# Performance work log

Measured on AMD Instinct MI355X. Metric: run time of the kernel, lower is better.

The kernel has to match this reference:

```python
import jax, jax.numpy as jnp
import numpy as np

HEADS = 16  # matches init_kwargs


def setup_inputs() -> dict:
    key = jax.random.key(0)
    ks = jax.random.split(key, 9)
    N, L, E, D = 2, 2048, 1024, 64
    return {
        "query": jax.random.normal(ks[0], (N, L, E), dtype=jnp.float32),
        "keys": jax.random.normal(ks[1], (N, L, E), dtype=jnp.float32),
        "values": jax.random.normal(ks[2], (N, L, E), dtype=jnp.float32),
        "masks": jax.random.randint(ks[3], (N, 1, 1, L), 0, 2, dtype=jnp.int32),
        "Wq": jax.random.normal(ks[4], (D, D), dtype=jnp.float32) / np.sqrt(D),
        "Wk": jax.random.normal(ks[5], (D, D), dtype=jnp.float32) / np.sqrt(D),
        "Wv": jax.random.normal(ks[6], (D, D), dtype=jnp.float32) / np.sqrt(D),
        "Wo": jax.random.normal(ks[7], (E, E), dtype=jnp.float32) / np.sqrt(E),
        "bo": jax.random.normal(ks[8], (E,), dtype=jnp.float32),
    }


def reference(query, keys, values, masks, Wq, Wk, Wv, Wo, bo):
    N, Lq, E = query.shape
    Lk = keys.shape[1]
    H = HEADS
    D = E // H
    # split heads: [N, L, H, D]
    q = query.reshape(N, Lq, H, D)
    k = keys.reshape(N, Lk, H, D)
    v = values.reshape(N, Lk, H, D)
    # per-head linear projections (weights shared across heads); Linear: x @ W.T
    q = jnp.einsum("nqhd,ed->nqhe", q, Wq)
    k = jnp.einsum("nkhd,ed->nkhe", k, Wk)
    v = jnp.einsum("nkhd,ed->nkhe", v, Wv)
    # scores [N, H, Lq, Lk]
    scores = jnp.einsum("nqhd,nkhd->nhqk", q, k)
    scores = jnp.where(masks == 0, jnp.float32(-1e20), scores)
    # NOTE: original scales by sqrt(embed_size), not sqrt(head_dim)
    attn = jax.nn.softmax(scores / jnp.sqrt(jnp.float32(E)), axis=3)
    out = jnp.einsum("nhqk,nkhd->nqhd", attn, v).reshape(N, Lq, E)
    return out @ Wo.T + bo
```

## Files before the change

### kernel.cpp

```cpp
#include <hip/hip_runtime.h>


typedef __bf16 bf16_t;
typedef __bf16 bf16x4 __attribute__((ext_vector_type(4)));
typedef __bf16 bf16x8 __attribute__((ext_vector_type(8)));
typedef float f32x4 __attribute__((ext_vector_type(4)));
typedef unsigned int u32x4 __attribute__((ext_vector_type(4)));

#define MFMA16(a, b, c) __builtin_amdgcn_mfma_f32_16x16x32_bf16((a), (b), (c), 0, 0, 0)

#define GLOAD_LDS16(gp, lp)                                              \
    __builtin_amdgcn_global_load_lds(                                    \
        (const __attribute__((address_space(1))) void*)(gp),             \
        (__attribute__((address_space(3))) void*)(lp), 16, 0, 0)

__device__ inline bf16x8 cvt8(const float* __restrict__ p, float scale) {
    f32x4 a = *(const f32x4*)p;
    f32x4 b = *(const f32x4*)(p + 4);
    bf16x8 r;
    r[0] = (bf16_t)(a[0] * scale); r[1] = (bf16_t)(a[1] * scale);
    r[2] = (bf16_t)(a[2] * scale); r[3] = (bf16_t)(a[3] * scale);
    r[4] = (bf16_t)(b[0] * scale); r[5] = (bf16_t)(b[1] * scale);
    r[6] = (bf16_t)(b[2] * scale); r[7] = (bf16_t)(b[3] * scale);
    return r;
}

__device__ inline bf16x8 cvt8s(const f32x4 a, const f32x4 b, float scale) {
    bf16x8 r;
    r[0] = (bf16_t)(a[0] * scale); r[1] = (bf16_t)(a[1] * scale);
    r[2] = (bf16_t)(a[2] * scale); r[3] = (bf16_t)(a[3] * scale);
    r[4] = (bf16_t)(b[0] * scale); r[5] = (bf16_t)(b[1] * scale);
    r[6] = (bf16_t)(b[2] * scale); r[7] = (bf16_t)(b[3] * scale);
    return r;
}

__device__ inline float exp2_fast(float x) {
    float r;
    asm("v_exp_f32 %0, %1" : "=v"(r) : "v"(x));
    return r;
}

__device__ inline unsigned cvt_pk_bf16(float lo, float hi) {
    unsigned r;
    asm("v_cvt_pk_bf16_f32 %0, %1, %2" : "=v"(r) : "v"(lo), "v"(hi));
    return r;
}

__device__ inline void xchg_quads(unsigned &x, unsigned &y) {
    asm("v_permlane32_swap_b32 %0, %1\n\t"
        "v_permlane16_swap_b32 %0, %1"
        : "+v"(x), "+v"(y));
}

__global__ __launch_bounds__(256) void scan_kernel(const int* __restrict__ msk,
                                                   int* __restrict__ excl)
{
    __shared__ int wsum[4];
    const int n = blockIdx.x;
    const int t = threadIdx.x, lane = t & 63, w = t >> 6;
    const int* m = msk + n * 2048;
    int* e = excl + n * 2049;

    int v[8], s = 0;
    #pragma unroll
    for (int j = 0; j < 8; j++) { v[j] = (m[t * 8 + j] != 0); s += v[j]; }

    int inc = s;
    #pragma unroll
    for (int d = 1; d < 64; d <<= 1) {
        int o = __shfl_up(inc, d);
        if (lane >= d) inc += o;
    }
    if (lane == 63) wsum[w] = inc;
    __syncthreads();
    int off = 0;
    #pragma unroll
    for (int i = 0; i < 4; i++)
        if (i < w) off += wsum[i];

    int a = off + inc - s;
    #pragma unroll
    for (int j = 0; j < 8; j++) { e[t * 8 + j] = a; a += v[j]; }
    if (t == 255) e[2048] = a;
}

__global__ __launch_bounds__(256) void qkv_proj_kernel(
    const float* __restrict__ qin, const float* __restrict__ kin,
    const float* __restrict__ vin,
    const float* __restrict__ Wq, const float* __restrict__ Wk,
    const float* __restrict__ Wv, const float* __restrict__ Wo,
    const int* __restrict__ excl,
    bf16_t* __restrict__ qp, bf16_t* __restrict__ kc, bf16_t* __restrict__ vcT,
    bf16_t* __restrict__ Wob)
{
    __shared__ __align__(16) char smem[51200];

    const int t = threadIdx.x;
    const int w = t >> 6, lane = t & 63, quad = lane >> 4, l16 = lane & 15;

    if (blockIdx.y == 3) {
        int idx = blockIdx.x * 1024 + t * 4;
        f32x4 v = *(const f32x4*)&Wo[idx];
        bf16x4 r;
        r[0] = (bf16_t)v[0]; r[1] = (bf16_t)v[1];
        r[2] = (bf16_t)v[2]; r[3] = (bf16_t)v[3];
        *(bf16x4*)&Wob[idx] = r;
        return;
    }

    if (blockIdx.y == 2) {
        bf16_t* Ct = (bf16_t*)smem;
        short* mapS = (short*)(smem + 16384);
        const int h = blockIdx.x & 15;
        const int tb = (blockIdx.x >> 4) * 64;
        const int n = tb >> 11, l0 = tb & 2047;
        const int tg = tb + w * 16 + l16;

        bf16x8 b0 = cvt8(&vin[(size_t)tg * 1024 + h * 64 + quad * 8], 1.0f);
        bf16x8 b1 = cvt8(&vin[(size_t)tg * 1024 + h * 64 + 32 + quad * 8], 1.0f);

        const int cbase = excl[n * 2049 + l0];
        const int cnt   = excl[n * 2049 + l0 + 64] - cbase;
        if (t < 64) {
            int c  = excl[n * 2049 + l0 + t];
            int c1 = excl[n * 2049 + l0 + t + 1];
            if (c1 > c) mapS[c - cbase] = (short)t;
        }

        #pragma unroll
        for (int nt = 0; nt < 4; nt++) {
            bf16x8 a0 = cvt8(&Wv[(nt * 16 + l16) * 64 + quad * 8], 1.0f);
            bf16x8 a1 = cvt8(&Wv[(nt * 16 + l16) * 64 + 32 + quad * 8], 1.0f);
            f32x4 acc = {0.f, 0.f, 0.f, 0.f};
            acc = MFMA16(a0, b0, acc);
            acc = MFMA16(a1, b1, acc);
            #pragma unroll
            for (int r = 0; r < 4; r++)
                Ct[(nt * 16 + quad * 4 + r) * 72 + w * 16 + l16] = (bf16_t)acc[r];
        }
        __syncthreads();
        const int p = t & 63, rg = t >> 6;
        if (p < cnt) {
            int j = mapS[p];
            size_t ob = ((size_t)(n * 16 + h)) * 131072 + cbase + p;
            #pragma unroll
            for (int rr = 0; rr < 16; rr++) {
                int r = rg * 16 + rr;
                vcT[ob + (size_t)r * 2048] = Ct[r * 72 + j];
            }
        }
        return;
    }

    if (blockIdx.x >= 512) return;
    const bool isK = (blockIdx.y == 1);
    const float* x; const float* W; float scale;
    if (!isK) { x = qin; W = Wq; scale = 0.04508422f; }
    else      { x = kin; W = Wk; scale = 1.0f; }

    float* Xs = (float*)smem;
    bf16_t* Ct2 = (bf16_t*)(smem + 32768);

    const int g0 = blockIdx.x * 128;

    #pragma unroll
    for (int j = 0; j < 8; j++) {
        int br = w * 32 + j * 4;
        int srow = br + (lane >> 4);
        int scol = ((lane & 15) ^ (srow & 15)) * 4;
        GLOAD_LDS16(&x[(size_t)(g0 + srow) * 64 + scol], &Xs[br * 64]);
    }
    __syncthreads();

    const int rbase = w * 32;
    bf16x8 a[2][2];
    #pragma unroll
    for (int qs = 0; qs < 2; qs++) {
        int row = rbase + qs * 16 + l16;
        const char* rowp = (const char*)Xs + (size_t)row * 256;
        int swb = (row & 15) << 4;
        #pragma unroll
        for (int c = 0; c < 2; c++) {
            f32x4 lo = *(const f32x4*)(rowp + ((c * 128 + quad * 32) ^ swb));
            f32x4 hi = *(const f32x4*)(rowp + ((c * 128 + quad * 32 + 16) ^ swb));
            a[qs][c] = cvt8s(lo, hi, scale);
        }
    }

    f32x4 acc[4][2];
    #pragma unroll
    for (int nt = 0; nt < 4; nt++) {
        bf16x8 b0 = cvt8(&W[(nt * 16 + l16) * 64 + quad * 8], 1.0f);
        bf16x8 b1 = cvt8(&W[(nt * 16 + l16) * 64 + 32 + quad * 8], 1.0f);
        #pragma unroll
        for (int qs = 0; qs < 2; qs++) {
            f32x4 z = {0.f, 0.f, 0.f, 0.f};
            z = MFMA16(a[qs][0], b0, z);
            z = MFMA16(a[qs][1], b1, z);
            acc[nt][qs] = z;
        }
    }

    #pragma unroll
    for (int nt = 0; nt < 4; nt++)
        #pragma unroll
        for (int qs = 0; qs < 2; qs++)
            #pragma unroll
            for (int r = 0; r < 4; r++)
                Ct2[(rbase + qs * 16 + quad * 4 + r) * 72 + nt * 16 + l16] = (bf16_t)acc[nt][qs][r];
    __syncthreads();

    #pragma unroll
    for (int it = 0; it < 4; it++) {
        int j = it * 32 + (t >> 3);
        int g = g0 + j, h2 = g & 15, token = g >> 4;
        int n2 = token >> 11, l = token & 2047;
        bf16x8 val = *(const bf16x8*)&Ct2[j * 72 + (t & 7) * 8];
        if (isK) {
            int c  = excl[n2 * 2049 + l];
            int c1 = excl[n2 * 2049 + l + 1];
            if (c1 > c)
                *(bf16x8*)&kc[(((size_t)(n2 * 16 + h2)) * 2048 + c) * 64 + (t & 7) * 8] = val;
        } else {
            *(bf16x8*)&qp[(((size_t)(n2 * 16 + h2)) * 2048 + l) * 64 + (t & 7) * 8] = val;
        }
    }
}

__global__ __launch_bounds__(256) void attn_kernel(
    const bf16_t* __restrict__ qp, const bf16_t* __restrict__ kc,
    const bf16_t* __restrict__ vcT, const int* __restrict__ excl,
    bf16_t* __restrict__ ao)
{
    __shared__ bf16_t Kt[2][64][64];
    __shared__ bf16_t Vt[2][64][64];

    const int t = threadIdx.x;
    const int w = t >> 6, lane = t & 63, quad = lane >> 4, l16 = lane & 15;

    const int flat = blockIdx.x;
    const int xcd = flat & 7, slot = flat >> 3;
    const int nh = xcd * 4 + (slot >> 4), qb = slot & 15;
    const int n = nh >> 4, h = nh & 15;
    const int qbase = qb * 128 + w * 32;
    const size_t nhbase = (size_t)nh * 131072;

    const int Lc = excl[n * 2049 + 2048];
    const int ntiles = (Lc + 63) >> 6;

    const int scol = ((lane & 7) ^ (lane >> 3)) * 8;
    const int swr  = l16 & 7;
    const int ck0  = (quad ^ swr) * 8;
    const int ck1  = ((quad + 4) ^ swr) * 8;

    bf16x8 aq[2][2];
    #pragma unroll
    for (int qs = 0; qs < 2; qs++)
        #pragma unroll
        for (int c = 0; c < 2; c++)
            aq[qs][c] = *(const bf16x8*)&qp[nhbase + (size_t)(qbase + qs * 16 + l16) * 64 + c * 32 + quad * 8];

    f32x4 o[2][4];
    float lsum[2] = {0.f, 0.f};
    #pragma unroll
    for (int qs = 0; qs < 2; qs++)
        #pragma unroll
        for (int dt = 0; dt < 4; dt++) {
            o[qs][dt][0] = 0.f; o[qs][dt][1] = 0.f; o[qs][dt][2] = 0.f; o[qs][dt][3] = 0.f;
        }

    const int kwbase = w * 16;

    #pragma unroll
    for (int j = 0; j < 2; j++) {
        int rb = kwbase + j * 8;
        GLOAD_LDS16(&kc[nhbase + (size_t)(rb + (lane >> 3)) * 64 + scol], &Kt[0][rb][0]);
        GLOAD_LDS16(&vcT[nhbase + (size_t)(rb + (lane >> 3)) * 2048 + scol], &Vt[0][rb][0]);
    }

    for (int i = 0; i < ntiles; i++) {
        const int cb = i & 1, nb = cb ^ 1;
        const int k0 = i * 64;
        __syncthreads();

        if (i + 1 < ntiles) {
            const int kn = k0 + 64;
            #pragma unroll
            for (int j = 0; j < 2; j++) {
                int rb = kwbase + j * 8;
                GLOAD_LDS16(&kc[nhbase + (size_t)(kn + rb + (lane >> 3)) * 64 + scol],
                            &Kt[nb][rb][0]);
                GLOAD_LDS16(&vcT[nhbase + (size_t)(rb + (lane >> 3)) * 2048 + kn + scol],
                            &Vt[nb][rb][0]);
            }
        }

        f32x4 st[2][4];
        #pragma unroll
        for (int ct = 0; ct < 4; ct++) {
            bf16x8 kb0 = *(const bf16x8*)&Kt[cb][ct * 16 + l16][ck0];
            bf16x8 kb1 = *(const bf16x8*)&Kt[cb][ct * 16 + l16][ck1];
            #pragma unroll
            for (int qs = 0; qs < 2; qs++) {
                f32x4 acc = {0.f, 0.f, 0.f, 0.f};
                acc = MFMA16(kb0, aq[qs][0], acc);
                acc = MFMA16(kb1, aq[qs][1], acc);
                st[qs][ct] = acc;
            }
        }

        if (k0 + 64 <= Lc) {
            #pragma unroll
            for (int qs = 0; qs < 2; qs++)
                #pragma unroll
                for (int ct = 0; ct < 4; ct++)
                    #pragma unroll
                    for (int r = 0; r < 4; r++) {
                        float p = exp2_fast(st[qs][ct][r]);
                        lsum[qs] += p;
                        st[qs][ct][r] = p;
                    }
        } else {
            #pragma unroll
            for (int qs = 0; qs < 2; qs++)
                #pragma unroll
                for (int ct = 0; ct < 4; ct++)
                    #pragma unroll
                    for (int r = 0; r < 4; r++) {
                        int kk = k0 + ct * 16 + quad * 4 + r;
                        float p = (kk < Lc) ? exp2_fast(st[qs][ct][r]) : 0.0f;
                        lsum[qs] += p;
                        st[qs][ct][r] = p;
                    }
        }

        bf16x8 bp[2][2];
        #pragma unroll
        for (int qs = 0; qs < 2; qs++) {
            unsigned u[4][2];
            #pragma unroll
            for (int ct = 0; ct < 4; ct++) {
                u[ct][0] = cvt_pk_bf16(st[qs][ct][0], st[qs][ct][1]);
                u[ct][1] = cvt_pk_bf16(st[qs][ct][2], st[qs][ct][3]);
            }
            #pragma unroll
            for (int hh = 0; hh < 2; hh++) {
                unsigned b0 = u[2 * hh][0], b2 = u[2 * hh + 1][0];
                xchg_quads(b0, b2);
                unsigned b1 = u[2 * hh][1], b3 = u[2 * hh + 1][1];
                xchg_quads(b1, b3);
                u32x4 q4 = {b0, b1, b2, b3};
                bp[qs][hh] = __builtin_bit_cast(bf16x8, q4);
            }
        }

        #pragma unroll
        for (int dt = 0; dt < 4; dt++) {
            bf16x8 va0 = *(const bf16x8*)&Vt[cb][dt * 16 + l16][ck0];
            bf16x8 va1 = *(const bf16x8*)&Vt[cb][dt * 16 + l16][ck1];
            #pragma unroll
            for (int qs = 0; qs < 2; qs++) {
                o[qs][dt] = MFMA16(va0, bp[qs][0], o[qs][dt]);
                o[qs][dt] = MFMA16(va1, bp[qs][1], o[qs][dt]);
            }
        }
    }

    #pragma unroll
    for (int qs = 0; qs < 2; qs++) {
        float v = lsum[qs];
        v += __shfl_xor(v, 16);
        v += __shfl_xor(v, 32);
        float inv = 1.0f / v;
        const int q = qbase + qs * 16 + l16;
        const size_t base = ((size_t)n * 2048 + q) * 1024 + h * 64;
        #pragma unroll
        for (int dt = 0; dt < 4; dt++) {
            bf16x4 ov;
            #pragma unroll
            for (int r = 0; r < 4; r++) ov[r] = (bf16_t)(o[qs][dt][r] * inv);
            *(bf16x4*)&ao[base + dt * 16 + quad * 4] = ov;
        }
    }
}

__global__ __launch_bounds__(256, 2) void out_proj_kernel(
    const bf16_t* __restrict__ X, const bf16_t* __restrict__ Wob,
    const float* __restrict__ bo, float* __restrict__ out)
{
    __shared__ bf16_t Xs[2][128][64];
    __shared__ bf16_t Ws[2][64][64];

    const int t = threadIdx.x;
    const int w = t >> 6, lane = t & 63, quad = lane >> 4, l16 = lane & 15;
    const int Mbase = blockIdx.x * 128;
    const int Nbase = blockIdx.y * 64;
    const int mrow = (w & 1) * 64;
    const int ncol = (w >> 1) * 32;

    const int scol = ((lane & 7) ^ (lane >> 3)) * 8;
    const int swr  = l16 & 7;

    f32x4 acc[4][2];
    #pragma unroll
    for (int mi = 0; mi < 4; mi++)
        #pragma unroll
        for (int ni = 0; ni < 2; ni++) {
            acc[mi][ni][0] = 0.f; acc[mi][ni][1] = 0.f;
            acc[mi][ni][2] = 0.f; acc[mi][ni][3] = 0.f;
        }

    #pragma unroll
    for (int j = 0; j < 4; j++) {
        int br = w * 32 + j * 8;
        GLOAD_LDS16(&X[(size_t)(Mbase + br + (lane >> 3)) * 1024 + scol], &Xs[0][br][0]);
    }
    #pragma unroll
    for (int j = 0; j < 2; j++) {
        int br = w * 16 + j * 8;
        GLOAD_LDS16(&Wob[(size_t)(Nbase + br + (lane >> 3)) * 1024 + scol], &Ws[0][br][0]);
    }

    for (int i = 0; i < 16; i++) {
        const int cb = i & 1, nb = cb ^ 1;
        __syncthreads();

        if (i < 15) {
            const int kn = (i + 1) * 64;
            #pragma unroll
            for (int j = 0; j < 4; j++) {
                int br = w * 32 + j * 8;
                GLOAD_LDS16(&X[(size_t)(Mbase + br + (lane >> 3)) * 1024 + kn + scol],
                            &Xs[nb][br][0]);
            }
            #pragma unroll
            for (int j = 0; j < 2; j++) {
                int br = w * 16 + j * 8;
                GLOAD_LDS16(&Wob[(size_t)(Nbase + br + (lane >> 3)) * 1024 + kn + scol],
                            &Ws[nb][br][0]);
            }
        }

        #pragma unroll
        for (int c = 0; c < 2; c++) {
            bf16x8 bfr[2];
            #pragma unroll
            for (int ni = 0; ni < 2; ni++)
                bfr[ni] = *(const bf16x8*)&Ws[cb][ncol + ni * 16 + l16][((c * 4 + quad) ^ swr) * 8];
            #pragma unroll
            for (int mi = 0; mi < 4; mi++) {
                bf16x8 afr = *(const bf16x8*)&Xs[cb][mrow + mi * 16 + l16][((c * 4 + quad) ^ swr) * 8];
                #pragma unroll
                for (int ni = 0; ni < 2; ni++)
                    acc[mi][ni] = MFMA16(afr, bfr[ni], acc[mi][ni]);
            }
        }
    }

    #pragma unroll
    for (int ni = 0; ni < 2; ni++) {
        float b = bo[Nbase + ncol + ni * 16 + l16];
        #pragma unroll
        for (int mi = 0; mi < 4; mi++) {
            #pragma unroll
            for (int r = 0; r < 4; r++) {
                int row = Mbase + mrow + mi * 16 + quad * 4 + r;
                out[(size_t)row * 1024 + Nbase + ncol + ni * 16 + l16] = acc[mi][ni][r] + b;
            }
        }
    }
}

extern "C" void kernel_launch(void* const* d_in, const int* in_sizes, int n_in,
                              void* d_out, int out_size, void* d_ws, size_t ws_size,
                              hipStream_t stream)
{
    const float* qin = (const float*)d_in[0];
    const float* kin = (const float*)d_in[1];
    const float* vin = (const float*)d_in[2];
    const int*   msk = (const int*)d_in[3];
    const float* Wq  = (const float*)d_in[4];
    const float* Wk  = (const float*)d_in[5];
    const float* Wv  = (const float*)d_in[6];
    const float* Wo  = (const float*)d_in[7];
    const float* bo  = (const float*)d_in[8];
    float* out = (float*)d_out;

    bf16_t* ws  = (bf16_t*)d_ws;
    bf16_t* qp  = ws;
    bf16_t* kc  = ws + 4194304;
    bf16_t* vcT = ws + 8388608;
    bf16_t* ao  = ws + 12582912;
    bf16_t* Wob = ws + 16777216;
    int* excl   = (int*)(ws + 17825792);

    scan_kernel<<<2, 256, 0, stream>>>(msk, excl);
    qkv_proj_kernel<<<dim3(1024, 4), 256, 0, stream>>>(qin, kin, vin, Wq, Wk, Wv, Wo,
                                                        excl, qp, kc, vcT, Wob);
    attn_kernel<<<dim3(512), 256, 0, stream>>>(qp, kc, vcT, excl, ao);
    out_proj_kernel<<<dim3(32, 16), 256, 0, stream>>>(ao, Wob, bo, out);
}
```

Before: 173.5 us.

## Gather only unmasked keys via index map and widen attention KV tiles

```diff
diff --git a/kernel.cpp b/kernel.cpp
--- a/kernel.cpp
+++ b/kernel.cpp
@@ -53,13 +53,15 @@
 }
 
 __global__ __launch_bounds__(256) void scan_kernel(const int* __restrict__ msk,
-                                                   int* __restrict__ excl)
+                                                   int* __restrict__ excl,
+                                                   int* __restrict__ lmap)
 {
     __shared__ int wsum[4];
     const int n = blockIdx.x;
     const int t = threadIdx.x, lane = t & 63, w = t >> 6;
     const int* m = msk + n * 2048;
     int* e = excl + n * 2049;
+    int* lm = lmap + n * 2048;
 
     int v[8], s = 0;
     #pragma unroll
@@ -80,7 +82,11 @@
 
     int a = off + inc - s;
     #pragma unroll
-    for (int j = 0; j < 8; j++) { e[t * 8 + j] = a; a += v[j]; }
+    for (int j = 0; j < 8; j++) {
+        e[t * 8 + j] = a;
+        if (v[j]) lm[a] = t * 8 + j;
+        a += v[j];
+    }
     if (t == 255) e[2048] = a;
 }
 
@@ -89,7 +95,7 @@
     const float* __restrict__ vin,
     const float* __restrict__ Wq, const float* __restrict__ Wk,
     const float* __restrict__ Wv, const float* __restrict__ Wo,
-    const int* __restrict__ excl,
+    const int* __restrict__ excl, const int* __restrict__ lmap,
     bf16_t* __restrict__ qp, bf16_t* __restrict__ kc, bf16_t* __restrict__ vcT,
     bf16_t* __restrict__ Wob)
 {
@@ -110,22 +116,20 @@
 
     if (blockIdx.y == 2) {
         bf16_t* Ct = (bf16_t*)smem;
-        short* mapS = (short*)(smem + 16384);
         const int h = blockIdx.x & 15;
-        const int tb = (blockIdx.x >> 4) * 64;
-        const int n = tb >> 11, l0 = tb & 2047;
-        const int tg = tb + w * 16 + l16;
-
-        bf16x8 b0 = cvt8(&vin[(size_t)tg * 1024 + h * 64 + quad * 8], 1.0f);
-        bf16x8 b1 = cvt8(&vin[(size_t)tg * 1024 + h * 64 + 32 + quad * 8], 1.0f);
-
-        const int cbase = excl[n * 2049 + l0];
-        const int cnt   = excl[n * 2049 + l0 + 64] - cbase;
-        if (t < 64) {
-            int c  = excl[n * 2049 + l0 + t];
-            int c1 = excl[n * 2049 + l0 + t + 1];
-            if (c1 > c) mapS[c - cbase] = (short)t;
-        }
+        const int ctile = blockIdx.x >> 4;
+        const int n = ctile >> 5;
+        const int c0 = (ctile & 31) * 64;
+        const int Lc = excl[n * 2049 + 2048];
+        if (c0 >= Lc) return;
+
+        const int p0 = w * 16 + l16;
+        int cs = c0 + p0; if (cs > Lc - 1) cs = Lc - 1;
+        const int tg = lmap[n * 2048 + cs];
+        const size_t rb = ((size_t)(n * 2048 + tg)) * 1024 + h * 64;
+
+        bf16x8 b0 = cvt8(&vin[rb + quad * 8], 1.0f);
+        bf16x8 b1 = cvt8(&vin[rb + 32 + quad * 8], 1.0f);
 
         #pragma unroll
         for (int nt = 0; nt < 4; nt++) {
@@ -140,13 +144,13 @@
         }
         __syncthreads();
         const int p = t & 63, rg = t >> 6;
+        const int cnt = (Lc - c0 < 64) ? (Lc - c0) : 64;
         if (p < cnt) {
-            int j = mapS[p];
-            size_t ob = ((size_t)(n * 16 + h)) * 131072 + cbase + p;
+            size_t ob = ((size_t)(n * 16 + h)) * 131072 + c0 + p;
             #pragma unroll
             for (int rr = 0; rr < 16; rr++) {
                 int r = rg * 16 + rr;
-                vcT[ob + (size_t)r * 2048] = Ct[r * 72 + j];
+                vcT[ob + (size_t)r * 2048] = Ct[r * 72 + p];
             }
         }
         return;
@@ -155,8 +159,15 @@
     if (blockIdx.x >= 512) return;
     const bool isK = (blockIdx.y == 1);
     const float* x; const float* W; float scale;
+    int n = 0, c0 = 0, Lc = 0;
     if (!isK) { x = qin; W = Wq; scale = 0.04508422f; }
-    else      { x = kin; W = Wk; scale = 1.0f; }
+    else {
+        x = kin; W = Wk; scale = 1.0f;
+        n = blockIdx.x >> 8;
+        c0 = (blockIdx.x & 255) * 8;
+        Lc = excl[n * 2049 + 2048];
+        if (c0 >= Lc) return;
+    }
 
     float* Xs = (float*)smem;
     bf16_t* Ct2 = (bf16_t*)(smem + 32768);
@@ -168,7 +179,16 @@
         int br = w * 32 + j * 4;
         int srow = br + (lane >> 4);
         int scol = ((lane & 15) ^ (srow & 15)) * 4;
-        GLOAD_LDS16(&x[(size_t)(g0 + srow) * 64 + scol], &Xs[br * 64]);
+        size_t gaddr;
+        if (!isK) {
+            gaddr = (size_t)(g0 + srow) * 64 + scol;
+        } else {
+            int csx = c0 + (srow >> 4); if (csx > Lc - 1) csx = Lc - 1;
+            int hs = srow & 15;
+            int ls = lmap[n * 2048 + csx];
+            gaddr = ((size_t)((n * 2048 + ls) * 16 + hs)) * 64 + scol;
+        }
+        GLOAD_LDS16(&x[gaddr], &Xs[br * 64]);
     }
     __syncthreads();
 
@@ -213,15 +233,14 @@
     #pragma unroll
     for (int it = 0; it < 4; it++) {
         int j = it * 32 + (t >> 3);
-        int g = g0 + j, h2 = g & 15, token = g >> 4;
-        int n2 = token >> 11, l = token & 2047;
         bf16x8 val = *(const bf16x8*)&Ct2[j * 72 + (t & 7) * 8];
         if (isK) {
-            int c  = excl[n2 * 2049 + l];
-            int c1 = excl[n2 * 2049 + l + 1];
-            if (c1 > c)
-                *(bf16x8*)&kc[(((size_t)(n2 * 16 + h2)) * 2048 + c) * 64 + (t & 7) * 8] = val;
+            int c = c0 + (j >> 4), h2 = j & 15;
+            if (c < Lc)
+                *(bf16x8*)&kc[(((size_t)(n * 16 + h2)) * 2048 + c) * 64 + (t & 7) * 8] = val;
         } else {
+            int g = g0 + j, h2 = g & 15, token = g >> 4;
+            int n2 = token >> 11, l = token & 2047;
             *(bf16x8*)&qp[(((size_t)(n2 * 16 + h2)) * 2048 + l) * 64 + (t & 7) * 8] = val;
         }
     }
@@ -232,8 +251,8 @@
     const bf16_t* __restrict__ vcT, const int* __restrict__ excl,
     bf16_t* __restrict__ ao)
 {
-    __shared__ bf16_t Kt[2][64][64];
-    __shared__ bf16_t Vt[2][64][64];
+    __shared__ bf16_t Kt[2][128][64];
+    __shared__ bf16_t Vt[2][64][128];
 
     const int t = threadIdx.x;
     const int w = t >> 6, lane = t & 63, quad = lane >> 4, l16 = lane & 15;
@@ -246,12 +265,13 @@
     const size_t nhbase = (size_t)nh * 131072;
 
     const int Lc = excl[n * 2049 + 2048];
-    const int ntiles = (Lc + 63) >> 6;
-
-    const int scol = ((lane & 7) ^ (lane >> 3)) * 8;
-    const int swr  = l16 & 7;
-    const int ck0  = (quad ^ swr) * 8;
-    const int ck1  = ((quad + 4) ^ swr) * 8;
+    const int ntiles = (Lc + 127) >> 7;
+
+    const int ksrow = lane >> 3;
+    const int kscol = ((lane & 7) ^ (lane >> 3)) * 8;
+    const int swr = l16 & 7;
+    const int ck0 = (quad ^ swr) * 8;
+    const int ck1 = ((quad + 4) ^ swr) * 8;
 
     bf16x8 aq[2][2];
     #pragma unroll
@@ -269,100 +289,110 @@
             o[qs][dt][0] = 0.f; o[qs][dt][1] = 0.f; o[qs][dt][2] = 0.f; o[qs][dt][3] = 0.f;
         }
 
-    const int kwbase = w * 16;
-
-    #pragma unroll
-    for (int j = 0; j < 2; j++) {
-        int rb = kwbase + j * 8;
-        GLOAD_LDS16(&kc[nhbase + (size_t)(rb + (lane >> 3)) * 64 + scol], &Kt[0][rb][0]);
-        GLOAD_LDS16(&vcT[nhbase + (size_t)(rb + (lane >> 3)) * 2048 + scol], &Vt[0][rb][0]);
-    }
+#define STAGE_KV(buf, kn)                                                     \
+    {                                                                         \
+        _Pragma("unroll")                                                     \
+        for (int j = 0; j < 4; j++) {                                         \
+            int rb = w * 32 + j * 8;                                          \
+            GLOAD_LDS16(&kc[nhbase + (size_t)((kn) + rb + ksrow) * 64 + kscol],\
+                        &Kt[buf][rb][0]);                                     \
+        }                                                                     \
+        _Pragma("unroll")                                                     \
+        for (int j = 0; j < 4; j++) {                                         \
+            int rb = w * 16 + j * 4;                                          \
+            int d = rb + (lane >> 4);                                         \
+            int sc = ((lane & 15) ^ (d & 15)) * 8;                            \
+            GLOAD_LDS16(&vcT[nhbase + (size_t)d * 2048 + (kn) + sc],          \
+                        &Vt[buf][rb][0]);                                     \
+        }                                                                     \
+    }
+
+    STAGE_KV(0, 0);
 
     for (int i = 0; i < ntiles; i++) {
         const int cb = i & 1, nb = cb ^ 1;
-        const int k0 = i * 64;
+        const int k0 = i * 128;
         __syncthreads();
 
-        if (i + 1 < ntiles) {
-            const int kn = k0 + 64;
-            #pragma unroll
-            for (int j = 0; j < 2; j++) {
-                int rb = kwbase + j * 8;
-                GLOAD_LDS16(&kc[nhbase + (size_t)(kn + rb + (lane >> 3)) * 64 + scol],
-                            &Kt[nb][rb][0]);
-                GLOAD_LDS16(&vcT[nhbase + (size_t)(rb + (lane >> 3)) * 2048 + kn + scol],
-                            &Vt[nb][rb][0]);
-            }
-        }
-
-        f32x4 st[2][4];
-        #pragma unroll
-        for (int ct = 0; ct < 4; ct++) {
-            bf16x8 kb0 = *(const bf16x8*)&Kt[cb][ct * 16 + l16][ck0];
-            bf16x8 kb1 = *(const bf16x8*)&Kt[cb][ct * 16 + l16][ck1];
+        if (i + 1 < ntiles) STAGE_KV(nb, k0 + 128);
+
+        #pragma unroll
+        for (int hf = 0; hf < 2; hf++) {
+            const int kh = k0 + hf * 64;
+
+            f32x4 st[2][4];
+            __builtin_amdgcn_s_setprio(1);
+            #pragma unroll
+            for (int ct = 0; ct < 4; ct++) {
+                bf16x8 kb0 = *(const bf16x8*)&Kt[cb][hf * 64 + ct * 16 + l16][ck0];
+                bf16x8 kb1 = *(const bf16x8*)&Kt[cb][hf * 64 + ct * 16 + l16][ck1];
+                #pragma unroll
+                for (int qs = 0; qs < 2; qs++) {
+                    f32x4 acc = {0.f, 0.f, 0.f, 0.f};
+                    acc = MFMA16(kb0, aq[qs][0], acc);
+                    acc = MFMA16(kb1, aq[qs][1], acc);
+                    st[qs][ct] = acc;
+                }
+            }
+            __builtin_amdgcn_s_setprio(0);
+
+            if (kh + 64 <= Lc) {
+                #pragma unroll
+                for (int qs = 0; qs < 2; qs++)
+                    #pragma unroll
+                    for (int ct = 0; ct < 4; ct++)
+                        #pragma unroll
+                        for (int r = 0; r < 4; r++) {
+                            float p = exp2_fast(st[qs][ct][r]);
+                            lsum[qs] += p;
+                            st[qs][ct][r] = p;
+                        }
+            } else {
+                #pragma unroll
+                for (int qs = 0; qs < 2; qs++)
+                    #pragma unroll
+                    for (int ct = 0; ct < 4; ct++)
+                        #pragma unroll
+                        for (int r = 0; r < 4; r++) {
+                            int kk = kh + ct * 16 + quad * 4 + r;
+                            float p = (kk < Lc) ? exp2_fast(st[qs][ct][r]) : 0.0f;
+                            lsum[qs] += p;
+                            st[qs][ct][r] = p;
+                        }
+            }
+
+            bf16x8 bp[2][2];
             #pragma unroll
             for (int qs = 0; qs < 2; qs++) {
-                f32x4 acc = {0.f, 0.f, 0.f, 0.f};
-                acc = MFMA16(kb0, aq[qs][0], acc);
-                acc = MFMA16(kb1, aq[qs][1], acc);
-                st[qs][ct] = acc;
-            }
-        }
-
-        if (k0 + 64 <= Lc) {
-            #pragma unroll
-            for (int qs = 0; qs < 2; qs++)
-                #pragma unroll
-                for (int ct = 0; ct < 4; ct++)
-                    #pragma unroll
-                    for (int r = 0; r < 4; r++) {
-                        float p = exp2_fast(st[qs][ct][r]);
-                        lsum[qs] += p;
-                        st[qs][ct][r] = p;
-                    }
-        } else {
-            #pragma unroll
-            for (int qs = 0; qs < 2; qs++)
-                #pragma unroll
-                for (int ct = 0; ct < 4; ct++)
-                    #pragma unroll
-                    for (int r = 0; r < 4; r++) {
-                        int kk = k0 + ct * 16 + quad * 4 + r;
-                        float p = (kk < Lc) ? exp2_fast(st[qs][ct][r]) : 0.0f;
-                        lsum[qs] += p;
-                        st[qs][ct][r] = p;
-                    }
-        }
-
-        bf16x8 bp[2][2];
-        #pragma unroll
-        for (int qs = 0; qs < 2; qs++) {
-            unsigned u[4][2];
-            #pragma unroll
-            for (int ct = 0; ct < 4; ct++) {
-                u[ct][0] = cvt_pk_bf16(st[qs][ct][0], st[qs][ct][1]);
-                u[ct][1] = cvt_pk_bf16(st[qs][ct][2], st[qs][ct][3]);
-            }
-            #pragma unroll
-            for (int hh = 0; hh < 2; hh++) {
-                unsigned b0 = u[2 * hh][0], b2 = u[2 * hh + 1][0];
-                xchg_quads(b0, b2);
-                unsigned b1 = u[2 * hh][1], b3 = u[2 * hh + 1][1];
-                xchg_quads(b1, b3);
-                u32x4 q4 = {b0, b1, b2, b3};
-                bp[qs][hh] = __builtin_bit_cast(bf16x8, q4);
-            }
-        }
-
-        #pragma unroll
-        for (int dt = 0; dt < 4; dt++) {
-            bf16x8 va0 = *(const bf16x8*)&Vt[cb][dt * 16 + l16][ck0];
-            bf16x8 va1 = *(const bf16x8*)&Vt[cb][dt * 16 + l16][ck1];
-            #pragma unroll
-            for (int qs = 0; qs < 2; qs++) {
-                o[qs][dt] = MFMA16(va0, bp[qs][0], o[qs][dt]);
-                o[qs][dt] = MFMA16(va1, bp[qs][1], o[qs][dt]);
-            }
+                unsigned u[4][2];
+                #pragma unroll
+                for (int ct = 0; ct < 4; ct++) {
+                    u[ct][0] = cvt_pk_bf16(st[qs][ct][0], st[qs][ct][1]);
+                    u[ct][1] = cvt_pk_bf16(st[qs][ct][2], st[qs][ct][3]);
+                }
+                #pragma unroll
+                for (int hh = 0; hh < 2; hh++) {
+                    unsigned b0 = u[2 * hh][0], b2 = u[2 * hh + 1][0];
+                    xchg_quads(b0, b2);
+                    unsigned b1 = u[2 * hh][1], b3 = u[2 * hh + 1][1];
+                    xchg_quads(b1, b3);
+                    u32x4 q4 = {b0, b1, b2, b3};
+                    bp[qs][hh] = __builtin_bit_cast(bf16x8, q4);
+                }
+            }
+
+            __builtin_amdgcn_s_setprio(1);
+            #pragma unroll
+            for (int dt = 0; dt < 4; dt++) {
+                bf16x8 va0 = *(const bf16x8*)&Vt[cb][dt * 16 + l16][((hf * 8 + quad) ^ l16) * 8];
+                bf16x8 va1 = *(const bf16x8*)&Vt[cb][dt * 16 + l16][((hf * 8 + 4 + quad) ^ l16) * 8];
+                #pragma unroll
+                for (int qs = 0; qs < 2; qs++) {
+                    o[qs][dt] = MFMA16(va0, bp[qs][0], o[qs][dt]);
+                    o[qs][dt] = MFMA16(va1, bp[qs][1], o[qs][dt]);
+                }
+            }
+            __builtin_amdgcn_s_setprio(0);
         }
     }
 
@@ -493,10 +523,11 @@
     bf16_t* ao  = ws + 12582912;
     bf16_t* Wob = ws + 16777216;
     int* excl   = (int*)(ws + 17825792);
-
-    scan_kernel<<<2, 256, 0, stream>>>(msk, excl);
+    int* lmap   = excl + 4100;
+
+    scan_kernel<<<2, 256, 0, stream>>>(msk, excl, lmap);
     qkv_proj_kernel<<<dim3(1024, 4), 256, 0, stream>>>(qin, kin, vin, Wq, Wk, Wv, Wo,
-                                                        excl, qp, kc, vcT, Wob);
+                                                        excl, lmap, qp, kc, vcT, Wob);
     attn_kernel<<<dim3(512), 256, 0, stream>>>(qp, kc, vcT, excl, ao);
     out_proj_kernel<<<dim3(32, 16), 256, 0, stream>>>(ao, Wob, bo, out);
 }
```

New measurement: 167.0 us. 1.04x faster.
